# Optimization experiments

Hardware: AMD Instinct MI355X
Metric: run time of the kernel (lower is better)

The kernel has to match this reference:

```python
import jax, jax.numpy as jnp
import numpy as np

LAMBDA_MIN = 0.1
LAMBDA_GLOBAL_MIN = 0.1
LAMBDA_GLOBAL_SCALE = 1.0
SLOPE = 0.2  # negative_slope


def leaky(x):
    return jnp.where(x >= 0, x, SLOPE * x)


def setup_inputs() -> dict:
    key = jax.random.key(0)
    ks = jax.random.split(key, 16)
    n, d, E, C, R = 10000, 128, 320000, 50000, 20
    s = 0.05
    h = jax.random.normal(ks[0], (n, d), jnp.float32)
    edge_index = jax.random.randint(ks[1], (2, E), 0, n)
    edge_type = jax.random.randint(ks[2], (E,), 0, R)
    rel_table = jax.random.normal(ks[3], (R, d), jnp.float32) * s
    # constraints taken from a subset of edges so matches exist
    constraint_indices = edge_index[:, :C]
    constraint_values = jax.random.normal(ks[4], (C,), jnp.float32)
    constraint_types = jax.random.randint(ks[5], (C,), 0, 4)
    att_in = 3 * d  # out*2 + in_dim (use_relation)
    W = jax.random.normal(ks[6], (d, d), jnp.float32) * s
    W_bi = jax.random.normal(ks[7], (d, d), jnp.float32) * s
    att_w1 = jax.random.normal(ks[8], (d, att_in), jnp.float32) * s
    att_b1 = jnp.zeros((d,), jnp.float32)
    att_w2 = jax.random.normal(ks[9], (d,), jnp.float32) * s
    gate_w1 = jax.random.normal(ks[10], (d, 2 * d), jnp.float32) * s
    gate_b1 = jnp.zeros((d,), jnp.float32)
    gate_w2 = jax.random.normal(ks[11], (d,), jnp.float32) * s
    gate_b2 = jnp.zeros((), jnp.float32)
    lambda_c = jnp.full((4,), 0.5, jnp.float32)  # CONSTRAINT_LAMBDA_INIT
    lambda_global = jnp.array(0.5, jnp.float32)
    return dict(h=h, edge_index=edge_index, edge_type=edge_type,
                rel_table=rel_table, constraint_indices=constraint_indices,
                constraint_values=constraint_values, constraint_types=constraint_types,
                W=W, W_bi=W_bi, att_w1=att_w1, att_b1=att_b1, att_w2=att_w2,
                gate_w1=gate_w1, gate_b1=gate_b1, gate_w2=gate_w2, gate_b2=gate_b2,
                lambda_c=lambda_c, lambda_global=lambda_global)


def reference(h, edge_index, edge_type, rel_table, constraint_indices,
              constraint_values, constraint_types, W, W_bi, att_w1, att_b1,
              att_w2, gate_w1, gate_b1, gate_w2, gate_b2, lambda_c, lambda_global):
    n = h.shape[0]
    Wh = h @ W.T                                  # [n, d]
    src, tgt = edge_index[0], edge_index[1]
    src_emb, tgt_emb = Wh[src], Wh[tgt]           # [E, d]
    r_emb = rel_table[edge_type]                  # [E, d]
    att_in = jnp.concatenate([src_emb, tgt_emb, r_emb], axis=-1)  # [E, 3d]
    e = leaky(att_in @ att_w1.T + att_b1) @ att_w2                # [E]

    # ---- constraints (bounded lambdas) ----
    lc = jax.nn.sigmoid(lambda_c) * (1.0 - LAMBDA_MIN) + LAMBDA_MIN
    lg = jax.nn.sigmoid(lambda_global) * (LAMBDA_GLOBAL_SCALE - LAMBDA_GLOBAL_MIN) + LAMBDA_GLOBAL_MIN
    ws = lc[constraint_types] * constraint_values                 # [C]
    c_keys = constraint_indices[0] * n + constraint_indices[1]
    e_keys = src * n + tgt
    # O(n^2) scatter buffers, faithful to the original
    c_agg = jnp.zeros((n * n,), jnp.float32).at[c_keys].add(ws)
    c_exists = jnp.zeros((n * n,), jnp.float32).at[c_keys].add(1.0)
    ms = c_agg[e_keys]
    mask = c_exists[e_keys] > 0
    ms = ms * mask.astype(jnp.float32)
    # constraint gate on matched edges (unmatched entries are 0 anyway)
    gi = jnp.concatenate([src_emb, tgt_emb], axis=-1)             # [E, 2d]
    g = jax.nn.sigmoid(leaky(gi @ gate_w1.T + gate_b1) @ gate_w2 + gate_b2)
    ms = jnp.where(mask, g * ms, ms)
    n_matched = mask.sum()
    global_bias = lg * jnp.mean(ws) * 0.01
    e = jnp.where(n_matched > 0, e + lg * ms, e + global_bias)

    # ---- scatter softmax over src neighborhoods ----
    mx = jax.ops.segment_max(e, src, num_segments=n)
    ex = jnp.exp(jnp.minimum(e - mx[src], 20.0))
    sm = jax.ops.segment_sum(ex, src, num_segments=n)
    attn = ex / (sm[src] + 1e-10)                                 # [E]

    # ---- weighted scatter-add aggregation ----
    side = jax.ops.segment_sum(attn[:, None] * tgt_emb, src, num_segments=n)  # [n, d]

    sum_out = leaky(Wh + side)
    bi_out = leaky((Wh * side) @ W_bi.T)
    h_new = sum_out + bi_out + Wh   # bi-interaction + residual
    return jax.nn.elu(h_new)
```

## Files before the change

kernel.cpp:

```cpp
#include <hip/hip_runtime.h>
#include <stdint.h>

#define SLOPE 0.2f
#define HASH_SIZE 131072
#define POIS ((int)0xAAAAAAAA)
#define MAXDEG 64

typedef __attribute__((ext_vector_type(8))) short bf16x8;
typedef __attribute__((ext_vector_type(4))) float f32x4;

__device__ __forceinline__ float leakyf(float x) { return fmaxf(x, SLOPE * x); }
__device__ __forceinline__ float sigmoidf(float x) { return 1.f / (1.f + __expf(-x)); }
__device__ __forceinline__ unsigned short f2bf(float f) {
  union { float f; unsigned int i; } c; c.f = f;
  unsigned int u = c.i;
  return (unsigned short)((u + 0x7fffu + ((u >> 16) & 1u)) >> 16);
}
__device__ __forceinline__ float bf2f(unsigned short u) {
  union { unsigned int i; float f; } c; c.i = ((unsigned int)u) << 16; return c.f;
}
__device__ __forceinline__ void unpk8(uint4 v, float* o) {
  union { unsigned int i; float f; } t;
  t.i = v.x << 16;          o[0] = t.f;
  t.i = v.x & 0xffff0000u;  o[1] = t.f;
  t.i = v.y << 16;          o[2] = t.f;
  t.i = v.y & 0xffff0000u;  o[3] = t.f;
  t.i = v.z << 16;          o[4] = t.f;
  t.i = v.z & 0xffff0000u;  o[5] = t.f;
  t.i = v.w << 16;          o[6] = t.f;
  t.i = v.w & 0xffff0000u;  o[7] = t.f;
}
__device__ __forceinline__ void ldbf8(const unsigned short* p, float* o) {
  unpk8(*(const uint4*)p, o);
}

__device__ __forceinline__ void mfma_core_a(const bf16x8 (&afr)[4],
                                            const unsigned short* bptr, f32x4 (&acc)[8]) {
  #pragma unroll
  for (int ks = 0; ks < 4; ++ks) {
    #pragma unroll
    for (int ct = 0; ct < 8; ++ct) {
      bf16x8 b = *(const bf16x8*)(bptr + ct * 2048 + ks * 32);
      acc[ct] = __builtin_amdgcn_mfma_f32_16x16x32_bf16(afr[ks], b, acc[ct], 0, 0, 0);
    }
  }
}

__global__ __launch_bounds__(256) void setup_kernel(
    const float* __restrict__ aw1, const float* __restrict__ gw1,
    const float* __restrict__ W, const float* __restrict__ Wbi,
    const float* __restrict__ rel, const float* __restrict__ ab1,
    const int* __restrict__ cidx, const float* __restrict__ cval,
    const int* __restrict__ ctype, const float* __restrict__ lc,
    unsigned short* __restrict__ Wcat, unsigned short* __restrict__ P3b16,
    int* __restrict__ hkeys,
    int C, int n, int R, int H)
{
  int i0 = blockIdx.x * blockDim.x + threadIdx.x;
  int stride = gridDim.x * blockDim.x;
  for (int j = i0; j < 6 * 16384; j += stride) {
    int mat = j >> 14, rest = j & 16383, col = rest >> 7, k = rest & 127;
    float v;
    switch (mat) {
      case 0:  v = aw1[col * 384 + k]; break;
      case 1:  v = aw1[col * 384 + 128 + k]; break;
      case 2:  v = gw1[col * 256 + k]; break;
      case 3:  v = gw1[col * 256 + 128 + k]; break;
      case 4:  v = W[col * 128 + k]; break;
      default: v = Wbi[col * 128 + k]; break;
    }
    Wcat[j] = f2bf(v);
  }
  for (int it = i0; it < R * 128; it += stride) {
    int r = it >> 7, jj = it & 127;
    float acc = ab1[jj];
    const float4* wrow = (const float4*)(aw1 + jj * 384 + 256);
    const float4* rl   = (const float4*)(rel + r * 128);
    #pragma unroll 8
    for (int k = 0; k < 32; ++k) {
      float4 a = rl[k], b = wrow[k];
      acc += a.x * b.x + a.y * b.y + a.z * b.z + a.w * b.w;
    }
    P3b16[it] = f2bf(acc);
  }
  for (int j = i0; j < C; j += stride) {
    int key = cidx[j] * n + cidx[C + j];
    float l = sigmoidf(lc[ctype[j]]) * 0.9f + 0.1f;
    float w = l * cval[j];
    unsigned int slot = ((unsigned int)key * 2654435761u) & (unsigned int)(H - 1);
    while (true) {
      int prev = atomicCAS(&hkeys[2 * slot], POIS, key);
      if (prev == POIS || prev == key) break;
      slot = (slot + 1) & (unsigned int)(H - 1);
    }
    atomicAdd((float*)&hkeys[2 * slot + 1], w);
  }
}

__device__ __forceinline__ void store_tile(const unsigned short (*t)[136],
                                           unsigned short* __restrict__ out,
                                           int rs, int rows_left, int lane)
{
  const int c = (lane & 15) * 8, q = lane >> 4;
  #pragma unroll
  for (int ro = 0; ro < 4; ++ro) {
    int row = ro * 4 + q;
    bf16x8 v = *(const bf16x8*)&t[row][c];
    if (row < rows_left)
      *(bf16x8*)(out + row * rs + c) = v;
  }
}

__global__ __launch_bounds__(256) void gemm_place(
    const int* __restrict__ ei, const int* __restrict__ etype,
    int* __restrict__ cursor, int2* __restrict__ trs2, int E,
    const float* __restrict__ h, const unsigned short* __restrict__ Wcat,
    const int2* __restrict__ hk,
    unsigned short* __restrict__ PW, unsigned short* __restrict__ PQ,
    unsigned short* __restrict__ Q2b,
    int n, int NB5, int H)
{
  if ((int)blockIdx.x >= NB5) {
    int i = ((int)blockIdx.x - NB5) * 256 + threadIdx.x;
    if (i < E) {
      int s = ei[i], t = ei[E + i], rt = etype[i];
      float ms = 0.f;
      int key = s * n + t;
      unsigned int slot = ((unsigned int)key * 2654435761u) & (unsigned int)(H - 1);
      while (true) {
        int2 kv = hk[slot];
        if (kv.x == key) { ms = __int_as_float(kv.y); break; }
        if (kv.x == POIS) break;
        slot = (slot + 1) & (unsigned int)(H - 1);
      }
      int k = atomicAdd(&cursor[s], 1) - POIS;
      if (k < MAXDEG)
        trs2[s * MAXDEG + k] = make_int2(t | (rt << 14), __float_as_int(ms));
    }
    return;
  }
  __shared__ unsigned short tile[4][16][136];
  const int wv = (int)threadIdx.x >> 6, lane = (int)threadIdx.x & 63;
  const int m0 = ((int)blockIdx.x * 4 + wv) * 16;
  if (m0 >= n) return;
  const int r = lane & 15, quad = lane >> 4;
  const int rows_left = n - m0;

  bf16x8 afr[4];
  const float* hrow = h + (size_t)min(m0 + r, n - 1) * 128 + quad * 8;
  #pragma unroll
  for (int ks = 0; ks < 4; ++ks) {
    float4 f0 = *(const float4*)(hrow + ks * 32);
    float4 f1 = *(const float4*)(hrow + ks * 32 + 4);
    bf16x8 a;
    a[0] = (short)f2bf(f0.x); a[1] = (short)f2bf(f0.y);
    a[2] = (short)f2bf(f0.z); a[3] = (short)f2bf(f0.w);
    a[4] = (short)f2bf(f1.x); a[5] = (short)f2bf(f1.y);
    a[6] = (short)f2bf(f1.z); a[7] = (short)f2bf(f1.w);
    afr[ks] = a;
  }

  f32x4 acc[8] = {};
  mfma_core_a(afr, Wcat + 4 * 16384 + r * 128 + quad * 8, acc);
  #pragma unroll
  for (int ct = 0; ct < 8; ++ct)
    #pragma unroll
    for (int rg = 0; rg < 4; ++rg)
      tile[wv][quad * 4 + rg][ct * 16 + r] = f2bf(acc[ct][rg]);

  bf16x8 wfr[4];
  #pragma unroll
  for (int ks = 0; ks < 4; ++ks)
    wfr[ks] = *(const bf16x8*)&tile[wv][r][quad * 8 + ks * 32];

  store_tile(tile[wv], PW + (size_t)m0 * 256 + 128, 256, rows_left, lane);

  #pragma unroll
  for (int mat = 0; mat < 4; ++mat) {
    f32x4 a2[8] = {};
    mfma_core_a(wfr, Wcat + mat * 16384 + r * 128 + quad * 8, a2);
    #pragma unroll
    for (int ct = 0; ct < 8; ++ct)
      #pragma unroll
      for (int rg = 0; rg < 4; ++rg)
        tile[wv][quad * 4 + rg][ct * 16 + r] = f2bf(a2[ct][rg]);
    unsigned short* out; int rs;
    if (mat == 0)      { out = PQ  + (size_t)m0 * 256;        rs = 256; }
    else if (mat == 1) { out = PW  + (size_t)m0 * 256;        rs = 256; }
    else if (mat == 2) { out = PQ  + (size_t)m0 * 256 + 128;  rs = 256; }
    else               { out = Q2b + (size_t)m0 * 128;        rs = 128; }
    store_tile(tile[wv], out, rs, rows_left, lane);
  }
}

__global__ __launch_bounds__(256) void fused_node_wave(
  const int* __restrict__ cursor,
  const int2* __restrict__ trs2,
  const unsigned short* __restrict__ PQ, const unsigned short* __restrict__ PW,
  const unsigned short* __restrict__ P3b16, const unsigned short* __restrict__ Q2,
  const float* __restrict__ aw2, const float* __restrict__ gb1,
  const float* __restrict__ gw2, const float* __restrict__ gb2,
  const float* __restrict__ lgp,
  float* __restrict__ side, unsigned short* __restrict__ Xb16, int n, int R)
{
  __shared__ unsigned short P3l[20 * 128];
  __shared__ int2  Bkt[2][MAXDEG];
  __shared__ float accl[2][16][8];
  __shared__ float sgl[2];

  const int tid  = (int)threadIdx.x;
  const int wv   = tid >> 6, lane = tid & 63;
  const int nl   = wv >> 1;
  const int hf   = wv & 1;
  const int g    = lane >> 4;
  const int u    = lane & 15;
  const int d0   = u * 8;
  const int gg   = hf * 4 + g;

  for (int j = tid; j < R * 64; j += 256)
    ((unsigned int*)P3l)[j] = ((const unsigned int*)P3b16)[j];

  const int node = (int)blockIdx.x * 2 + nl;
  int cnt = 0;
  if (node < n) {
    cnt = min(cursor[node] - POIS, MAXDEG);
    if (hf == 0) Bkt[nl][lane] = trs2[(size_t)node * MAXDEG + lane];
  }
  __syncthreads();

  float sg = 0.f;
  float acc[8] = {};

  if (node < n) {
    float p1v[8], w2v[8], qbv[8], g2v[8];
    const unsigned short* pqrow = PQ + (size_t)node * 256 + d0;
    ldbf8(pqrow, p1v);
    { float q1t[8]; ldbf8(pqrow + 128, q1t);
      float4 bA = *(const float4*)(gb1 + d0), bB = *(const float4*)(gb1 + d0 + 4);
      qbv[0]=q1t[0]+bA.x; qbv[1]=q1t[1]+bA.y; qbv[2]=q1t[2]+bA.z; qbv[3]=q1t[3]+bA.w;
      qbv[4]=q1t[4]+bB.x; qbv[5]=q1t[5]+bB.y; qbv[6]=q1t[6]+bB.z; qbv[7]=q1t[7]+bB.w; }
    { float4 a = *(const float4*)(aw2 + d0), b = *(const float4*)(aw2 + d0 + 4);
      w2v[0]=a.x; w2v[1]=a.y; w2v[2]=a.z; w2v[3]=a.w;
      w2v[4]=b.x; w2v[5]=b.y; w2v[6]=b.z; w2v[7]=b.w; }
    { float4 a = *(const float4*)(gw2 + d0), b = *(const float4*)(gw2 + d0 + 4);
      g2v[0]=a.x; g2v[1]=a.y; g2v[2]=a.z; g2v[3]=a.w;
      g2v[4]=b.x; g2v[5]=b.y; g2v[6]=b.z; g2v[7]=b.w; }
    float gb2s = gb2[0];
    float lg = sigmoidf(lgp[0]) * 0.9f + 0.1f;

    const int iters = (cnt + 7) >> 3;
    const int last = cnt - 1;

    auto consume = [&](float ms, uint4 rpa, uint4 rcc, uint4 rwv, uint4 rq2, bool active) {
      float pa[8], cc[8];
      unpk8(rpa, pa);
      unpk8(rcc, cc);
      float s = 0.f;
      #pragma unroll
      for (int d = 0; d < 8; ++d) s += leakyf(p1v[d] + pa[d] + cc[d]) * w2v[d];
      #pragma unroll
      for (int d = 1; d < 16; d <<= 1) s += __shfl_xor(s, d, 64);

      if (ms != 0.f) {
        float q2[8];
        unpk8(rq2, q2);
        float gp = 0.f;
        #pragma unroll
        for (int d = 0; d < 8; ++d) gp += leakyf(qbv[d] + q2[d]) * g2v[d];
        #pragma unroll
        for (int d = 1; d < 16; d <<= 1) gp += __shfl_xor(gp, d, 64);
        s += lg * (sigmoidf(gp + gb2s) * ms);
      }
      if (active) {
        float wvv[8];
        unpk8(rwv, wvv);
        float p = __expf(s);
        sg += p;
        #pragma unroll
        for (int d = 0; d < 8; ++d) acc[d] += p * wvv[d];
      }
    };

    int i = 0;
    for (; i + 2 <= iters; i += 2) {
      const int e0 = i * 8 + gg, e1 = e0 + 8;
      int2 t0 = Bkt[nl][min(e0, last)];
      int2 t1 = Bkt[nl][min(e1, last)];
      const int tx0 = t0.x & 16383, rt0 = (t0.x >> 14) & 31;
      const int tx1 = t1.x & 16383, rt1 = (t1.x >> 14) & 31;
      const unsigned short* pw0 = PW + (size_t)tx0 * 256 + d0;
      const unsigned short* pw1 = PW + (size_t)tx1 * 256 + d0;
      uint4 rpa0 = *(const uint4*)pw0;
      uint4 rwv0 = *(const uint4*)(pw0 + 128);
      uint4 rcc0 = *(const uint4*)&P3l[rt0 * 128 + d0];
      uint4 rq20 = make_uint4(0u, 0u, 0u, 0u);
      if (t0.y != 0) rq20 = *(const uint4*)(Q2 + (size_t)tx0 * 128 + d0);
      uint4 rpa1 = *(const uint4*)pw1;
      uint4 rwv1 = *(const uint4*)(pw1 + 128);
      uint4 rcc1 = *(const uint4*)&P3l[rt1 * 128 + d0];
      uint4 rq21 = make_uint4(0u, 0u, 0u, 0u);
      if (t1.y != 0) rq21 = *(const uint4*)(Q2 + (size_t)tx1 * 128 + d0);
      consume(__int_as_float(t0.y), rpa0, rcc0, rwv0, rq20, e0 < cnt);
      consume(__int_as_float(t1.y), rpa1, rcc1, rwv1, rq21, e1 < cnt);
    }
    for (; i < iters; ++i) {
      const int e0 = i * 8 + gg;
      int2 t0 = Bkt[nl][min(e0, last)];
      const int tx0 = t0.x & 16383, rt0 = (t0.x >> 14) & 31;
      const unsigned short* pw0 = PW + (size_t)tx0 * 256 + d0;
      uint4 rpa0 = *(const uint4*)pw0;
      uint4 rwv0 = *(const uint4*)(pw0 + 128);
      uint4 rcc0 = *(const uint4*)&P3l[rt0 * 128 + d0];
      uint4 rq20 = make_uint4(0u, 0u, 0u, 0u);
      if (t0.y != 0) rq20 = *(const uint4*)(Q2 + (size_t)tx0 * 128 + d0);
      consume(__int_as_float(t0.y), rpa0, rcc0, rwv0, rq20, e0 < cnt);
    }

    sg += __shfl_xor(sg, 16, 64);
    sg += __shfl_xor(sg, 32, 64);
    #pragma unroll
    for (int d = 0; d < 8; ++d) {
      acc[d] += __shfl_xor(acc[d], 16, 64);
      acc[d] += __shfl_xor(acc[d], 32, 64);
    }
    if (hf == 1 && g == 0) {
      *(f32x4*)&accl[nl][u][0] = *(const f32x4*)&acc[0];
      *(f32x4*)&accl[nl][u][4] = *(const f32x4*)&acc[4];
      if (u == 0) sgl[nl] = sg;
    }
  }
  __syncthreads();

  if (node < n && hf == 0 && g == 0) {
    sg += sgl[nl];
    #pragma unroll
    for (int d = 0; d < 8; ++d) acc[d] += accl[nl][u][d];

    float inv = 1.f / (sg + 1e-10f);
    int idx = node * 128 + d0;
    float wh[8];
    ldbf8(PW + (size_t)node * 256 + 128 + d0, wh);
    float4 sA = make_float4(acc[0]*inv, acc[1]*inv, acc[2]*inv, acc[3]*inv);
    float4 sB = make_float4(acc[4]*inv, acc[5]*inv, acc[6]*inv, acc[7]*inv);
    *(float4*)(side + idx) = sA;
    *(float4*)(side + idx + 4) = sB;
    ushort4 xA, xB;
    xA.x = f2bf(wh[0] * sA.x); xA.y = f2bf(wh[1] * sA.y);
    xA.z = f2bf(wh[2] * sA.z); xA.w = f2bf(wh[3] * sA.w);
    xB.x = f2bf(wh[4] * sB.x); xB.y = f2bf(wh[5] * sB.y);
    xB.z = f2bf(wh[6] * sB.z); xB.w = f2bf(wh[7] * sB.w);
    *(ushort4*)(Xb16 + idx) = xA;
    *(ushort4*)(Xb16 + idx + 4) = xB;
  }
}

__global__ __launch_bounds__(256) void final_kernel(
    const unsigned short* __restrict__ Xb16, const unsigned short* __restrict__ Wcat,
    int n, const unsigned short* __restrict__ PW, const float* __restrict__ side,
    float* __restrict__ outp)
{
  const int unit = (int)blockIdx.x * 4 + ((int)threadIdx.x >> 6);
  const int tile = unit >> 1, half = unit & 1;
  const int m0 = tile * 16;
  if (m0 >= n) return;
  const int lane = (int)threadIdx.x & 63;
  const int r = lane & 15, quad = lane >> 4;
  int arow = min(m0 + r, n - 1);

  bf16x8 afr[4];
  #pragma unroll
  for (int ks = 0; ks < 4; ++ks)
    afr[ks] = *(const bf16x8*)(Xb16 + (size_t)arow * 128 + quad * 8 + ks * 32);

  const unsigned short* bbase = Wcat + 5 * 16384 + (half * 4) * 2048 + r * 128 + quad * 8;
  f32x4 acc[4] = {};
  #pragma unroll
  for (int ks = 0; ks < 4; ++ks)
    #pragma unroll
    for (int ct = 0; ct < 4; ++ct) {
      bf16x8 b = *(const bf16x8*)(bbase + ct * 2048 + ks * 32);
      acc[ct] = __builtin_amdgcn_mfma_f32_16x16x32_bf16(afr[ks], b, acc[ct], 0, 0, 0);
    }
  #pragma unroll
  for (int ct = 0; ct < 4; ++ct) {
    #pragma unroll
    for (int rg = 0; rg < 4; ++rg) {
      int row = m0 + quad * 4 + rg;
      if (row >= n) continue;
      int col = (half * 4 + ct) * 16 + r;
      int idx = row * 128 + col;
      float v = acc[ct][rg];
      float w = bf2f(PW[(size_t)row * 256 + 128 + col]), s = side[idx];
      float hn = leakyf(w + s) + leakyf(v) + w;
      outp[idx] = hn > 0.f ? hn : __expf(hn) - 1.f;
    }
  }
}

extern "C" void kernel_launch(void* const* d_in, const int* in_sizes, int n_in,
                              void* d_out, int out_size, void* d_ws, size_t ws_size,
                              hipStream_t stream)
{
  const float* h    = (const float*)d_in[0];
  const int* ei     = (const int*)d_in[1];
  const int* etype  = (const int*)d_in[2];
  const float* rel  = (const float*)d_in[3];
  const int* cidx   = (const int*)d_in[4];
  const float* cval = (const float*)d_in[5];
  const int* ctype  = (const int*)d_in[6];
  const float* W    = (const float*)d_in[7];
  const float* Wbi  = (const float*)d_in[8];
  const float* aw1  = (const float*)d_in[9];
  const float* ab1  = (const float*)d_in[10];
  const float* aw2  = (const float*)d_in[11];
  const float* gw1  = (const float*)d_in[12];
  const float* gb1  = (const float*)d_in[13];
  const float* gw2  = (const float*)d_in[14];
  const float* gb2  = (const float*)d_in[15];
  const float* lc   = (const float*)d_in[16];
  const float* lgp  = (const float*)d_in[17];

  const int n = in_sizes[0] / 128;
  const int E = in_sizes[2];
  const int C = in_sizes[6];
  const int R = in_sizes[3] / 128;
  const int H = HASH_SIZE;

  char* ws = (char*)d_ws;
  size_t off = 0;
  auto alloc = [&](size_t bytes) -> void* {
    void* p = ws + off;
    off = (off + bytes + 255) & ~(size_t)255;
    return p;
  };
  unsigned short* PW    = (unsigned short*)alloc((size_t)n * 256 * 2);
  unsigned short* PQ    = (unsigned short*)alloc((size_t)n * 256 * 2);
  unsigned short* Q2b   = (unsigned short*)alloc((size_t)n * 128 * 2);
  unsigned short* Xb16  = (unsigned short*)alloc((size_t)n * 128 * 2);
  unsigned short* Wcat  = (unsigned short*)alloc((size_t)6 * 128 * 128 * 2);
  unsigned short* P3b16 = (unsigned short*)alloc((size_t)R * 128 * 2);
  float* side  = (float*)alloc((size_t)n * 128 * 4);
  int2* trs2   = (int2*)alloc((size_t)n * MAXDEG * 8);
  int* cursor  = (int*)alloc((size_t)n * 4);
  int* hki     = (int*)alloc((size_t)H * 8);
  (void)ws_size; (void)n_in; (void)out_size;

  const int NB5 = (n + 63) / 64;
  const int NBP = (E + 255) / 256;
  const int NBF = (n + 1) / 2;
  const int NBX = (2 * ((n + 15) / 16) + 3) / 4;

  setup_kernel<<<512, 256, 0, stream>>>(aw1, gw1, W, Wbi, rel, ab1,
                                        cidx, cval, ctype, lc,
                                        Wcat, P3b16, hki, C, n, R, H);
  gemm_place<<<NB5 + NBP, 256, 0, stream>>>(ei, etype, cursor, trs2, E,
                                            h, Wcat, (const int2*)hki,
                                            PW, PQ, Q2b, n, NB5, H);
  fused_node_wave<<<NBF, 256, 0, stream>>>(cursor, trs2, PQ, PW, P3b16, Q2b,
                                           aw2, gb1, gw2, gb2, lgp,
                                           side, Xb16, n, R);
  final_kernel<<<NBX, 256, 0, stream>>>(Xb16, Wcat, n, PW, side, (float*)d_out);
}
```

Baseline: 188.2 us.

## Assign one wave per node with register-held bucket and software-pipelined gathers

The node-aggregation kernel now maps one 64-lane wave to each node (four nodes per block) instead of two waves per node. This removes the cross-wave LDS reduction and the second block barrier. Bucket entries are held in registers and broadcast with shuffles instead of staged in LDS, and the edge loop is software-pipelined: the next edge's gathers are issued before the current one is consumed. The trade-off is fewer edges in flight per node and possibly higher register pressure from the staged loads.

```diff
diff --git a/kernel.cpp b/kernel.cpp
--- a/kernel.cpp
+++ b/kernel.cpp
@@ -204,138 +204,108 @@
   float* __restrict__ side, unsigned short* __restrict__ Xb16, int n, int R)
 {
   __shared__ unsigned short P3l[20 * 128];
-  __shared__ int2  Bkt[2][MAXDEG];
-  __shared__ float accl[2][16][8];
-  __shared__ float sgl[2];
-
-  const int tid  = (int)threadIdx.x;
-  const int wv   = tid >> 6, lane = tid & 63;
-  const int nl   = wv >> 1;
-  const int hf   = wv & 1;
-  const int g    = lane >> 4;
-  const int u    = lane & 15;
-  const int d0   = u * 8;
-  const int gg   = hf * 4 + g;
-
-  for (int j = tid; j < R * 64; j += 256)
+  for (int j = threadIdx.x; j < R * 64; j += 256)
     ((unsigned int*)P3l)[j] = ((const unsigned int*)P3b16)[j];
-
-  const int node = (int)blockIdx.x * 2 + nl;
-  int cnt = 0;
-  if (node < n) {
-    cnt = min(cursor[node] - POIS, MAXDEG);
-    if (hf == 0) Bkt[nl][lane] = trs2[(size_t)node * MAXDEG + lane];
-  }
   __syncthreads();
+
+  const int wv = (int)threadIdx.x >> 6;
+  const int lane = (int)threadIdx.x & 63;
+  const int g = lane >> 4;
+  const int u = lane & 15;
+  const int d0 = u * 8;
+
+  const int node = (int)blockIdx.x * 4 + wv;
+  if (node >= n) return;
+  const int cnt = min(cursor[node] - POIS, MAXDEG);
+  const int2 ment = trs2[(size_t)node * MAXDEG + lane];
+
+  float p1v[8], w2v[8], qbv[8], g2v[8];
+  const unsigned short* pqrow = PQ + (size_t)node * 256 + d0;
+  ldbf8(pqrow, p1v);
+  { float q1t[8]; ldbf8(pqrow + 128, q1t);
+    float4 bA = *(const float4*)(gb1 + d0), bB = *(const float4*)(gb1 + d0 + 4);
+    qbv[0]=q1t[0]+bA.x; qbv[1]=q1t[1]+bA.y; qbv[2]=q1t[2]+bA.z; qbv[3]=q1t[3]+bA.w;
+    qbv[4]=q1t[4]+bB.x; qbv[5]=q1t[5]+bB.y; qbv[6]=q1t[6]+bB.z; qbv[7]=q1t[7]+bB.w; }
+  { float4 a = *(const float4*)(aw2 + d0), b = *(const float4*)(aw2 + d0 + 4);
+    w2v[0]=a.x; w2v[1]=a.y; w2v[2]=a.z; w2v[3]=a.w;
+    w2v[4]=b.x; w2v[5]=b.y; w2v[6]=b.z; w2v[7]=b.w; }
+  { float4 a = *(const float4*)(gw2 + d0), b = *(const float4*)(gw2 + d0 + 4);
+    g2v[0]=a.x; g2v[1]=a.y; g2v[2]=a.z; g2v[3]=a.w;
+    g2v[4]=b.x; g2v[5]=b.y; g2v[6]=b.z; g2v[7]=b.w; }
+  float gb2s = gb2[0];
+  float lg = sigmoidf(lgp[0]) * 0.9f + 0.1f;
 
   float sg = 0.f;
   float acc[8] = {};
-
-  if (node < n) {
-    float p1v[8], w2v[8], qbv[8], g2v[8];
-    const unsigned short* pqrow = PQ + (size_t)node * 256 + d0;
-    ldbf8(pqrow, p1v);
-    { float q1t[8]; ldbf8(pqrow + 128, q1t);
-      float4 bA = *(const float4*)(gb1 + d0), bB = *(const float4*)(gb1 + d0 + 4);
-      qbv[0]=q1t[0]+bA.x; qbv[1]=q1t[1]+bA.y; qbv[2]=q1t[2]+bA.z; qbv[3]=q1t[3]+bA.w;
-      qbv[4]=q1t[4]+bB.x; qbv[5]=q1t[5]+bB.y; qbv[6]=q1t[6]+bB.z; qbv[7]=q1t[7]+bB.w; }
-    { float4 a = *(const float4*)(aw2 + d0), b = *(const float4*)(aw2 + d0 + 4);
-      w2v[0]=a.x; w2v[1]=a.y; w2v[2]=a.z; w2v[3]=a.w;
-      w2v[4]=b.x; w2v[5]=b.y; w2v[6]=b.z; w2v[7]=b.w; }
-    { float4 a = *(const float4*)(gw2 + d0), b = *(const float4*)(gw2 + d0 + 4);
-      g2v[0]=a.x; g2v[1]=a.y; g2v[2]=a.z; g2v[3]=a.w;
-      g2v[4]=b.x; g2v[5]=b.y; g2v[6]=b.z; g2v[7]=b.w; }
-    float gb2s = gb2[0];
-    float lg = sigmoidf(lgp[0]) * 0.9f + 0.1f;
-
-    const int iters = (cnt + 7) >> 3;
-    const int last = cnt - 1;
-
-    auto consume = [&](float ms, uint4 rpa, uint4 rcc, uint4 rwv, uint4 rq2, bool active) {
-      float pa[8], cc[8];
-      unpk8(rpa, pa);
-      unpk8(rcc, cc);
-      float s = 0.f;
+  const int iters = (cnt + 3) >> 2;
+  const int last = cnt - 1;
+
+  struct Stage { uint4 rpa, rwv, rcc, rq2; float ms; bool act; };
+
+  auto issue = [&](int e0) -> Stage {
+    Stage st;
+    int e = min(e0, last);
+    int bx = __shfl(ment.x, e, 64);
+    int by = __shfl(ment.y, e, 64);
+    int tx = bx & 16383, rt = (bx >> 14) & 31;
+    const unsigned short* pw = PW + (size_t)tx * 256 + d0;
+    st.rpa = *(const uint4*)pw;
+    st.rwv = *(const uint4*)(pw + 128);
+    st.rcc = *(const uint4*)&P3l[rt * 128 + d0];
+    st.rq2 = make_uint4(0u, 0u, 0u, 0u);
+    if (by != 0) st.rq2 = *(const uint4*)(Q2 + (size_t)tx * 128 + d0);
+    st.ms = __int_as_float(by);
+    st.act = e0 < cnt;
+    return st;
+  };
+
+  auto consume = [&](const Stage& st) {
+    float pa[8], cc[8];
+    unpk8(st.rpa, pa);
+    unpk8(st.rcc, cc);
+    float s = 0.f;
+    #pragma unroll
+    for (int d = 0; d < 8; ++d) s += leakyf(p1v[d] + pa[d] + cc[d]) * w2v[d];
+    #pragma unroll
+    for (int d = 1; d < 16; d <<= 1) s += __shfl_xor(s, d, 64);
+
+    if (st.ms != 0.f) {
+      float q2[8];
+      unpk8(st.rq2, q2);
+      float gp = 0.f;
       #pragma unroll
-      for (int d = 0; d < 8; ++d) s += leakyf(p1v[d] + pa[d] + cc[d]) * w2v[d];
+      for (int d = 0; d < 8; ++d) gp += leakyf(qbv[d] + q2[d]) * g2v[d];
       #pragma unroll
-      for (int d = 1; d < 16; d <<= 1) s += __shfl_xor(s, d, 64);
-
-      if (ms != 0.f) {
-        float q2[8];
-        unpk8(rq2, q2);
-        float gp = 0.f;
-        #pragma unroll
-        for (int d = 0; d < 8; ++d) gp += leakyf(qbv[d] + q2[d]) * g2v[d];
-        #pragma unroll
-        for (int d = 1; d < 16; d <<= 1) gp += __shfl_xor(gp, d, 64);
-        s += lg * (sigmoidf(gp + gb2s) * ms);
-      }
-      if (active) {
-        float wvv[8];
-        unpk8(rwv, wvv);
-        float p = __expf(s);
-        sg += p;
-        #pragma unroll
-        for (int d = 0; d < 8; ++d) acc[d] += p * wvv[d];
-      }
-    };
-
-    int i = 0;
-    for (; i + 2 <= iters; i += 2) {
-      const int e0 = i * 8 + gg, e1 = e0 + 8;
-      int2 t0 = Bkt[nl][min(e0, last)];
-      int2 t1 = Bkt[nl][min(e1, last)];
-      const int tx0 = t0.x & 16383, rt0 = (t0.x >> 14) & 31;
-      const int tx1 = t1.x & 16383, rt1 = (t1.x >> 14) & 31;
-      const unsigned short* pw0 = PW + (size_t)tx0 * 256 + d0;
-      const unsigned short* pw1 = PW + (size_t)tx1 * 256 + d0;
-      uint4 rpa0 = *(const uint4*)pw0;
-      uint4 rwv0 = *(const uint4*)(pw0 + 128);
-      uint4 rcc0 = *(const uint4*)&P3l[rt0 * 128 + d0];
-      uint4 rq20 = make_uint4(0u, 0u, 0u, 0u);
-      if (t0.y != 0) rq20 = *(const uint4*)(Q2 + (size_t)tx0 * 128 + d0);
-      uint4 rpa1 = *(const uint4*)pw1;
-      uint4 rwv1 = *(const uint4*)(pw1 + 128);
-      uint4 rcc1 = *(const uint4*)&P3l[rt1 * 128 + d0];
-      uint4 rq21 = make_uint4(0u, 0u, 0u, 0u);
-      if (t1.y != 0) rq21 = *(const uint4*)(Q2 + (size_t)tx1 * 128 + d0);
-      consume(__int_as_float(t0.y), rpa0, rcc0, rwv0, rq20, e0 < cnt);
-      consume(__int_as_float(t1.y), rpa1, rcc1, rwv1, rq21, e1 < cnt);
-    }
-    for (; i < iters; ++i) {
-      const int e0 = i * 8 + gg;
-      int2 t0 = Bkt[nl][min(e0, last)];
-      const int tx0 = t0.x & 16383, rt0 = (t0.x >> 14) & 31;
-      const unsigned short* pw0 = PW + (size_t)tx0 * 256 + d0;
-      uint4 rpa0 = *(const uint4*)pw0;
-      uint4 rwv0 = *(const uint4*)(pw0 + 128);
-      uint4 rcc0 = *(const uint4*)&P3l[rt0 * 128 + d0];
-      uint4 rq20 = make_uint4(0u, 0u, 0u, 0u);
-      if (t0.y != 0) rq20 = *(const uint4*)(Q2 + (size_t)tx0 * 128 + d0);
-      consume(__int_as_float(t0.y), rpa0, rcc0, rwv0, rq20, e0 < cnt);
-    }
-
-    sg += __shfl_xor(sg, 16, 64);
-    sg += __shfl_xor(sg, 32, 64);
-    #pragma unroll
-    for (int d = 0; d < 8; ++d) {
-      acc[d] += __shfl_xor(acc[d], 16, 64);
-      acc[d] += __shfl_xor(acc[d], 32, 64);
-    }
-    if (hf == 1 && g == 0) {
-      *(f32x4*)&accl[nl][u][0] = *(const f32x4*)&acc[0];
-      *(f32x4*)&accl[nl][u][4] = *(const f32x4*)&acc[4];
-      if (u == 0) sgl[nl] = sg;
-    }
-  }
-  __syncthreads();
-
-  if (node < n && hf == 0 && g == 0) {
-    sg += sgl[nl];
-    #pragma unroll
-    for (int d = 0; d < 8; ++d) acc[d] += accl[nl][u][d];
-
+      for (int d = 1; d < 16; d <<= 1) gp += __shfl_xor(gp, d, 64);
+      s += lg * (sigmoidf(gp + gb2s) * st.ms);
+    }
+    if (st.act) {
+      float wvv[8];
+      unpk8(st.rwv, wvv);
+      float p = __expf(s);
+      sg += p;
+      #pragma unroll
+      for (int d = 0; d < 8; ++d) acc[d] += p * wvv[d];
+    }
+  };
+
+  Stage A = issue(g);
+  for (int i = 0; i < iters; ++i) {
+    Stage B;
+    if (i + 1 < iters) B = issue((i + 1) * 4 + g);
+    consume(A);
+    A = B;
+  }
+
+  sg += __shfl_xor(sg, 16, 64);
+  sg += __shfl_xor(sg, 32, 64);
+  #pragma unroll
+  for (int d = 0; d < 8; ++d) {
+    acc[d] += __shfl_xor(acc[d], 16, 64);
+    acc[d] += __shfl_xor(acc[d], 32, 64);
+  }
+
+  if (g == 0) {
     float inv = 1.f / (sg + 1e-10f);
     int idx = node * 128 + d0;
     float wh[8];
@@ -447,7 +417,7 @@
 
   const int NB5 = (n + 63) / 64;
   const int NBP = (E + 255) / 256;
-  const int NBF = (n + 1) / 2;
+  const int NB4 = (n + 3) / 4;
   const int NBX = (2 * ((n + 15) / 16) + 3) / 4;
 
   setup_kernel<<<512, 256, 0, stream>>>(aw1, gw1, W, Wbi, rel, ab1,
@@ -456,7 +426,7 @@
   gemm_place<<<NB5 + NBP, 256, 0, stream>>>(ei, etype, cursor, trs2, E,
                                             h, Wcat, (const int2*)hki,
                                             PW, PQ, Q2b, n, NB5, H);
-  fused_node_wave<<<NBF, 256, 0, stream>>>(cursor, trs2, PQ, PW, P3b16, Q2b,
+  fused_node_wave<<<NB4, 256, 0, stream>>>(cursor, trs2, PQ, PW, P3b16, Q2b,
                                            aw2, gb1, gw2, gb2, lgp,
                                            side, Xb16, n, R);
   final_kernel<<<NBX, 256, 0, stream>>>(Xb16, Wcat, n, PW, side, (float*)d_out);
```

Result: no change. 186.2 us (-1.0%).
